# Optimization experiments

Measured on AMD Instinct MI355X. Metric: run time of the kernel, lower is better.

## Reference

```python
import jax, jax.numpy as jnp
import numpy as np

RADIUS = 0.4
NSAMPLE = 32
NORMALIZE_DP = True


def setup_inputs() -> dict:
    key = jax.random.key(0)
    k1, k2, k3 = jax.random.split(key, 3)
    B, N, K, C = 2, 16384, 4096, 128
    xyz = jax.random.normal(k1, (B, N, 3), dtype=jnp.float32)
    new_xyz = jax.random.normal(k2, (B, K, 3), dtype=jnp.float32)
    features = jax.random.normal(k3, (B, C, N), dtype=jnp.float32)
    return {"xyz": xyz, "new_xyz": new_xyz, "features": features}


def _ball_query(radius, nsample, xyz, new_xyz):
    # xyz: (B,N,3), new_xyz: (B,K,3) -> indices (B,K,nsample) int32
    N = xyz.shape[1]
    # squared distances via ||a||^2 + ||b||^2 - 2 a.b  -> (B,K,N)
    d2 = (jnp.sum(new_xyz * new_xyz, -1)[:, :, None]
          + jnp.sum(xyz * xyz, -1)[:, None, :]
          - 2.0 * jnp.einsum('bkd,bnd->bkn', new_xyz, xyz))
    mask = d2 < radius * radius
    # key = point index if inside ball else N (sentinel); take nsample smallest
    key = jnp.where(mask, jnp.arange(N, dtype=jnp.int32), jnp.int32(N))
    neg_top, _ = jax.lax.top_k(-key, nsample)  # (B,K,nsample)
    idx = -neg_top
    # pointnet2 semantics: pad with first in-radius index (0 if ball empty)
    first = idx[..., :1]
    first = jnp.where(first < N, first, 0)
    idx = jnp.where(idx < N, idx, first)
    return idx


def _group(features, idx):
    # features: (B,C,N), idx: (B,K,ns) -> (B,C,K,ns)
    return jax.vmap(lambda f, i: f[:, i])(features, idx)


def reference(xyz, new_xyz, features):
    idx = _ball_query(RADIUS, NSAMPLE, xyz, new_xyz)          # (B,K,ns)
    xyz_t = jnp.transpose(xyz, (0, 2, 1))                      # (B,3,N)
    grouped_xyz = _group(xyz_t, idx)                           # (B,3,K,ns)
    grouped_xyz = grouped_xyz - jnp.transpose(new_xyz, (0, 2, 1))[..., None]
    if NORMALIZE_DP:
        grouped_xyz = grouped_xyz / RADIUS
    grouped_features = _group(features, idx)                   # (B,C,K,ns)
    return (grouped_xyz, grouped_features)
```

## Files before the change

### kernel.cpp

```cpp
#include <hip/hip_runtime.h>

#define BB 2
#define NN 16384
#define KK 4096
#define CC 128
#define SS 32
#define BKK (BB * KK)

typedef float vfloat4 __attribute__((ext_vector_type(4)));

__global__ __launch_bounds__(256) void transpose_prep_kernel(
    const float* __restrict__ feat, const float* __restrict__ xyz,
    float* __restrict__ feat_t, float* __restrict__ xyzw)
{
    __shared__ float tile[64][133];
    const int b  = blockIdx.x >> 8;
    const int n0 = (blockIdx.x & 255) * 64;
    const int t  = threadIdx.x;

    if (t < 64) {
        const int i = b * NN + n0 + t;
        const float* p = xyz + (size_t)i * 3;
        const float x = p[0], y = p[1], z = p[2];
        const float pp = __fadd_rn(__fadd_rn(__fmul_rn(x, x), __fmul_rn(y, y)),
                                   __fmul_rn(z, z));
        vfloat4 v = {x, y, z, pp};
        *(vfloat4*)(xyzw + (size_t)i * 4) = v;
    }

#pragma unroll
    for (int i = 0; i < 8; ++i) {
        const int li = i * 256 + t;
        const int c  = li >> 4;
        const int n4 = (li & 15) * 4;
        const vfloat4 v = *(const vfloat4*)(feat + ((size_t)b * CC + c) * NN + n0 + n4);
        tile[n4 + 0][c] = v.x;
        tile[n4 + 1][c] = v.y;
        tile[n4 + 2][c] = v.z;
        tile[n4 + 3][c] = v.w;
    }
    __syncthreads();

#pragma unroll
    for (int i = 0; i < 8; ++i) {
        const int li = i * 256 + t;
        const int n  = li >> 5;
        const int c4 = (li & 31) * 4;
        vfloat4 v;
        v.x = tile[n][c4 + 0];
        v.y = tile[n][c4 + 1];
        v.z = tile[n][c4 + 2];
        v.w = tile[n][c4 + 3];
        *(vfloat4*)(feat_t + ((size_t)(b * NN + n0 + n)) * CC + c4) = v;
    }
}

__global__ __launch_bounds__(1024) void qsort_kernel(
    const float* __restrict__ new_xyz,
    int* __restrict__ qmap)
{
    __shared__ int hist[128];
    __shared__ int base[128];
    __shared__ unsigned char bk[BKK];

    const int t = threadIdx.x;
    if (t < 128) hist[t] = 0;
    __syncthreads();

#pragma unroll
    for (int c = 0; c < BKK / 1024; ++c) {
        const int q = c * 1024 + t;
        const int b = q >> 12;
        const float* p = new_xyz + (size_t)q * 3;
        const float qq = p[0] * p[0] + p[1] * p[1] + p[2] * p[2];
        int bkt = (int)(qq * 8.0f);
        bkt = bkt > 63 ? 63 : bkt;
        bkt |= (b << 6);
        bk[q] = (unsigned char)bkt;
        atomicAdd(&hist[bkt], 1);
    }
    __syncthreads();

    if (t == 0) {
        int s = 0;
#pragma unroll
        for (int i = 0; i < 128; ++i) { base[i] = s; s += hist[i]; }
    }
    __syncthreads();

#pragma unroll
    for (int c = 0; c < BKK / 1024; ++c) {
        const int q = c * 1024 + t;
        const int pos = atomicAdd(&base[bk[q]], 1);
        qmap[pos] = q;
    }
}

__global__ __launch_bounds__(256) void ball_query_kernel(
    const float* __restrict__ xyzw,
    const float* __restrict__ new_xyz,
    const int* __restrict__ qmap,
    int* __restrict__ idx_buf)
{
    __shared__ vfloat4 pts[256];

    const int t    = threadIdx.x;
    const int wave = t >> 6;
    const int lane = t & 63;
    const int qi   = qmap[blockIdx.x * 4 + wave];
    const int b    = qi >> 12;
    const int k    = qi & (KK - 1);

    const float R2 = (float)(0.4 * 0.4);

    const float* q = new_xyz + (size_t)(b * KK + k) * 3;
    const float qx = q[0], qy = q[1], qz = q[2];
    const float qq = __fadd_rn(__fadd_rn(__fmul_rn(qx, qx), __fmul_rn(qy, qy)),
                               __fmul_rn(qz, qz));

    const vfloat4* xw = (const vfloat4*)xyzw + (size_t)b * NN;
    int* out = idx_buf + (size_t)qi * SS;

    int cnt = 0;

    pts[t] = xw[t];
    __syncthreads();

    for (int base = 0; base < NN; base += 256) {
        const int nb = (base + 256 < NN) ? base + 256 : 0;
        const vfloat4 nxt = xw[nb + t];

        if (cnt < SS) {
            vfloat4 v0 = pts[lane];
            vfloat4 v1 = pts[64 + lane];
            vfloat4 v2 = pts[128 + lane];
            vfloat4 v3 = pts[192 + lane];

            auto d2test = [&](vfloat4 v) -> bool {
                const float dot = __fadd_rn(
                    __fadd_rn(__fmul_rn(qx, v.x), __fmul_rn(qy, v.y)),
                    __fmul_rn(qz, v.z));
                const float d2 = __fsub_rn(__fadd_rn(qq, v.w), __fmul_rn(2.0f, dot));
                return d2 < R2;
            };

            const bool i0 = d2test(v0);
            const bool i1 = d2test(v1);
            const bool i2 = d2test(v2);
            const bool i3 = d2test(v3);
            const unsigned long long m0 = __ballot(i0);
            const unsigned long long m1 = __ballot(i1);
            const unsigned long long m2 = __ballot(i2);
            const unsigned long long m3 = __ballot(i3);

            const int c0 = cnt;
            const int p0 = __popcll(m0), p1 = __popcll(m1);
            const int p2 = __popcll(m2), p3 = __popcll(m3);
            cnt = c0 + p0 + p1 + p2 + p3;

            if ((m0 | m1 | m2 | m3) != 0ull && c0 < SS) {
                const unsigned long long lt = (1ull << lane) - 1ull;
                int bs = c0;
                if (i0) { const int pos = bs + __popcll(m0 & lt);
                          if (pos < SS) out[pos] = base + lane; }
                bs += p0;
                if (i1) { const int pos = bs + __popcll(m1 & lt);
                          if (pos < SS) out[pos] = base + 64 + lane; }
                bs += p1;
                if (i2) { const int pos = bs + __popcll(m2 & lt);
                          if (pos < SS) out[pos] = base + 128 + lane; }
                bs += p2;
                if (i3) { const int pos = bs + __popcll(m3 & lt);
                          if (pos < SS) out[pos] = base + 192 + lane; }
            }
        }

        if (__syncthreads_and(cnt >= SS)) break;

        pts[t] = nxt;
        __syncthreads();
    }

    const int fill = (cnt > 0) ? out[0] : 0;
    if (lane < SS && lane >= cnt) out[lane] = fill;
}

__global__ __launch_bounds__(256) void group_kernel(
    const float* __restrict__ xyzw,
    const float* __restrict__ new_xyz,
    const float* __restrict__ feat_t,
    const int*   __restrict__ idx_buf,
    float* __restrict__ out)
{
    __shared__ float tile[SS * CC];
    __shared__ float txyz[3][SS];

    const int t    = threadIdx.x;
    const int l    = t & 63;
    const int w    = t >> 6;
    const int bk   = blockIdx.x;
    const int b    = bk >> 12;
    const int k    = bk & (KK - 1);
    const int half = l >> 5;
    const int cl   = l & 31;

#pragma unroll
    for (int p = 0; p < 4; ++p) {
        const int r = 8 * w + 2 * p;
        const int s = r + half;
        const int n = idx_buf[bk * SS + s];
        const int chunk = cl ^ ((s >> 2) & 7);
        const float* src = feat_t + ((size_t)(b * NN + n)) * CC + 4 * chunk;
        __builtin_amdgcn_global_load_lds(
            (const __attribute__((address_space(1))) void*)src,
            (__attribute__((address_space(3))) void*)(tile + r * CC),
            16, 0, 0);
    }

    if (t < SS) {
        const int n = idx_buf[bk * SS + t];
        const float* q = new_xyz + (size_t)bk * 3;
        const vfloat4 wv = *((const vfloat4*)xyzw + (size_t)b * NN + n);
        txyz[0][t] = (wv.x - q[0]) / 0.4f;
        txyz[1][t] = (wv.y - q[1]) / 0.4f;
        txyz[2][t] = (wv.z - q[2]) / 0.4f;
    }

    __syncthreads();

    float* out_xyz  = out;
    float* out_feat = out + (size_t)BB * 3 * KK * SS;

    const int sq = t & 7;
    const int c0 = t >> 3;
#pragma unroll
    for (int p = 0; p < 4; ++p) {
        const int c  = c0 + 32 * p;
        const int co = (((c >> 2) ^ sq) << 2) + (c & 3);
        vfloat4 v;
        v.x = tile[(4 * sq + 0) * CC + co];
        v.y = tile[(4 * sq + 1) * CC + co];
        v.z = tile[(4 * sq + 2) * CC + co];
        v.w = tile[(4 * sq + 3) * CC + co];
        __builtin_nontemporal_store(
            v, (vfloat4*)(out_feat + (((size_t)(b * CC + c) * KK + k) * SS + 4 * sq)));
    }

    if (t < 24) {
        const int d   = t >> 3;
        const int sq2 = t & 7;
        const vfloat4 v = *(vfloat4*)&txyz[d][4 * sq2];
        __builtin_nontemporal_store(
            v, (vfloat4*)(out_xyz + (((size_t)(b * 3 + d) * KK + k) * SS + 4 * sq2)));
    }
}

extern "C" void kernel_launch(void* const* d_in, const int* in_sizes, int n_in,
                              void* d_out, int out_size, void* d_ws, size_t ws_size,
                              hipStream_t stream) {
    const float* xyz     = (const float*)d_in[0];
    const float* new_xyz = (const float*)d_in[1];
    const float* feat    = (const float*)d_in[2];
    float* out = (float*)d_out;

    int*   idx_buf = (int*)d_ws;
    float* xyzw    = (float*)((char*)d_ws + (1 << 20));
    float* feat_t  = (float*)((char*)d_ws + (1 << 20) + (512 << 10));
    int*   qmap    = (int*)((char*)d_ws + (1 << 20) + (512 << 10) + (CC * NN * BB) * 4);

    transpose_prep_kernel<<<dim3(BB * (NN / 64)), dim3(256), 0, stream>>>(
        feat, xyz, feat_t, xyzw);

    qsort_kernel<<<dim3(1), dim3(1024), 0, stream>>>(new_xyz, qmap);

    ball_query_kernel<<<dim3(BKK / 4), dim3(256), 0, stream>>>(
        xyzw, new_xyz, qmap, idx_buf);

    group_kernel<<<dim3(BKK), dim3(256), 0, stream>>>(
        xyzw, new_xyz, feat_t, idx_buf, out);
}
```

Baseline: 99.91 us.

## Process four queries per wave in ball query, dropping shared-memory staging and block syncs

Each wavefront now handles four sorted (spatially nearby) queries at once, reusing every loaded point for four distance tests. Points are read straight from global memory into registers with a one-step prefetch, replacing the LDS tile and block-wide barriers. Each wave stops on its own once all four of its queries have filled. The first in-ball index is tracked in a register instead of being read back from memory. The cost is more registers, and a wave keeps scanning until its slowest query finishes. Queries in one wave are assumed to share a batch, which holds because the sorted groups never cross a batch boundary.

```diff
diff --git a/kernel.cpp b/kernel.cpp
--- a/kernel.cpp
+++ b/kernel.cpp
@@ -102,87 +102,66 @@
     const int* __restrict__ qmap,
     int* __restrict__ idx_buf)
 {
-    __shared__ vfloat4 pts[256];
-
-    const int t    = threadIdx.x;
-    const int wave = t >> 6;
-    const int lane = t & 63;
-    const int qi   = qmap[blockIdx.x * 4 + wave];
-    const int b    = qi >> 12;
-    const int k    = qi & (KK - 1);
+    const int wave = threadIdx.x >> 6;
+    const int lane = threadIdx.x & 63;
+    const int wq   = (blockIdx.x * 4 + wave) * 4;
 
     const float R2 = (float)(0.4 * 0.4);
 
-    const float* q = new_xyz + (size_t)(b * KK + k) * 3;
-    const float qx = q[0], qy = q[1], qz = q[2];
-    const float qq = __fadd_rn(__fadd_rn(__fmul_rn(qx, qx), __fmul_rn(qy, qy)),
-                               __fmul_rn(qz, qz));
-
+    int   qi[4];
+    float qx[4], qy[4], qz[4], qq[4];
+    int*  out[4];
+#pragma unroll
+    for (int j = 0; j < 4; ++j) {
+        qi[j] = qmap[wq + j];
+        const float* q = new_xyz + (size_t)qi[j] * 3;
+        qx[j] = q[0]; qy[j] = q[1]; qz[j] = q[2];
+        qq[j] = __fadd_rn(__fadd_rn(__fmul_rn(qx[j], qx[j]), __fmul_rn(qy[j], qy[j])),
+                          __fmul_rn(qz[j], qz[j]));
+        out[j] = idx_buf + (size_t)qi[j] * SS;
+    }
+    const int b = qi[0] >> 12;
     const vfloat4* xw = (const vfloat4*)xyzw + (size_t)b * NN;
-    int* out = idx_buf + (size_t)qi * SS;
-
-    int cnt = 0;
-
-    pts[t] = xw[t];
-    __syncthreads();
-
-    for (int base = 0; base < NN; base += 256) {
-        const int nb = (base + 256 < NN) ? base + 256 : 0;
-        const vfloat4 nxt = xw[nb + t];
-
-        if (cnt < SS) {
-            vfloat4 v0 = pts[lane];
-            vfloat4 v1 = pts[64 + lane];
-            vfloat4 v2 = pts[128 + lane];
-            vfloat4 v3 = pts[192 + lane];
-
-            auto d2test = [&](vfloat4 v) -> bool {
+
+    int cnt[4]   = {0, 0, 0, 0};
+    int first[4] = {-1, -1, -1, -1};
+
+    vfloat4 cur = xw[lane];
+    for (int base = 0; base < NN; base += 64) {
+        const int nb = (base + 64 < NN) ? base + 64 : 0;
+        const vfloat4 nxt = xw[nb + lane];
+
+        bool done = true;
+#pragma unroll
+        for (int j = 0; j < 4; ++j) {
+            if (cnt[j] < SS) {
                 const float dot = __fadd_rn(
-                    __fadd_rn(__fmul_rn(qx, v.x), __fmul_rn(qy, v.y)),
-                    __fmul_rn(qz, v.z));
-                const float d2 = __fsub_rn(__fadd_rn(qq, v.w), __fmul_rn(2.0f, dot));
-                return d2 < R2;
-            };
-
-            const bool i0 = d2test(v0);
-            const bool i1 = d2test(v1);
-            const bool i2 = d2test(v2);
-            const bool i3 = d2test(v3);
-            const unsigned long long m0 = __ballot(i0);
-            const unsigned long long m1 = __ballot(i1);
-            const unsigned long long m2 = __ballot(i2);
-            const unsigned long long m3 = __ballot(i3);
-
-            const int c0 = cnt;
-            const int p0 = __popcll(m0), p1 = __popcll(m1);
-            const int p2 = __popcll(m2), p3 = __popcll(m3);
-            cnt = c0 + p0 + p1 + p2 + p3;
-
-            if ((m0 | m1 | m2 | m3) != 0ull && c0 < SS) {
-                const unsigned long long lt = (1ull << lane) - 1ull;
-                int bs = c0;
-                if (i0) { const int pos = bs + __popcll(m0 & lt);
-                          if (pos < SS) out[pos] = base + lane; }
-                bs += p0;
-                if (i1) { const int pos = bs + __popcll(m1 & lt);
-                          if (pos < SS) out[pos] = base + 64 + lane; }
-                bs += p1;
-                if (i2) { const int pos = bs + __popcll(m2 & lt);
-                          if (pos < SS) out[pos] = base + 128 + lane; }
-                bs += p2;
-                if (i3) { const int pos = bs + __popcll(m3 & lt);
-                          if (pos < SS) out[pos] = base + 192 + lane; }
+                    __fadd_rn(__fmul_rn(qx[j], cur.x), __fmul_rn(qy[j], cur.y)),
+                    __fmul_rn(qz[j], cur.z));
+                const float d2 = __fsub_rn(__fadd_rn(qq[j], cur.w),
+                                           __fmul_rn(2.0f, dot));
+                const bool inball = d2 < R2;
+                const unsigned long long m = __ballot(inball);
+                if (m) {
+                    if (first[j] < 0) first[j] = base + (int)__builtin_ctzll(m);
+                    if (inball) {
+                        const int pos = cnt[j] + __popcll(m & ((1ull << lane) - 1ull));
+                        if (pos < SS) out[j][pos] = base + lane;
+                    }
+                    cnt[j] += __popcll(m);
+                }
             }
+            done = done && (cnt[j] >= SS);
         }
-
-        if (__syncthreads_and(cnt >= SS)) break;
-
-        pts[t] = nxt;
-        __syncthreads();
-    }
-
-    const int fill = (cnt > 0) ? out[0] : 0;
-    if (lane < SS && lane >= cnt) out[lane] = fill;
+        if (done) break;
+        cur = nxt;
+    }
+
+#pragma unroll
+    for (int j = 0; j < 4; ++j) {
+        const int fill = (first[j] < 0) ? 0 : first[j];
+        if (lane < SS && lane >= cnt[j]) out[j][lane] = fill;
+    }
 }
 
 __global__ __launch_bounds__(256) void group_kernel(
@@ -273,7 +252,7 @@
 
     qsort_kernel<<<dim3(1), dim3(1024), 0, stream>>>(new_xyz, qmap);
 
-    ball_query_kernel<<<dim3(BKK / 4), dim3(256), 0, stream>>>(
+    ball_query_kernel<<<dim3(BKK / 16), dim3(256), 0, stream>>>(
         xyzw, new_xyz, qmap, idx_buf);
 
     group_kernel<<<dim3(BKK), dim3(256), 0, stream>>>(
```

Measured after the change: 126.8 us. 1.27x slower.
